# Optimization experiments

Hardware: AMD Instinct MI355X
Metric: run time of the kernel (lower is better)

The kernel has to match this reference:

```python
import jax, jax.numpy as jnp
import numpy as np

N_NODES = 100000
N_EDGES = 600000
D = 128
H = 256


def setup_inputs() -> dict:
    key = jax.random.key(0)
    ks = jax.random.split(key, 8)
    nodes = jax.random.normal(ks[0], (N_NODES, D), dtype=jnp.float32)
    senders = jax.random.randint(ks[1], (N_EDGES,), 0, N_NODES)
    receivers = jax.random.randint(ks[2], (N_EDGES,), 0, N_NODES)
    s = 0.05
    return {
        "nodes": nodes,
        "senders": senders,
        "receivers": receivers,
        "Wm1": jax.random.normal(ks[3], (D, H), dtype=jnp.float32) * s,
        "bm1": jnp.zeros((H,), dtype=jnp.float32),
        "Wm2": jax.random.normal(ks[4], (H, D), dtype=jnp.float32) * s,
        "bm2": jnp.zeros((D,), dtype=jnp.float32),
        "Wn1": jax.random.normal(ks[5], (2 * D, H), dtype=jnp.float32) * s,
        "bn1": jnp.zeros((H,), dtype=jnp.float32),
        "Wn2": jax.random.normal(ks[6], (H, D), dtype=jnp.float32) * s,
        "bn2": jnp.zeros((D,), dtype=jnp.float32),
    }


def reference(nodes, senders, receivers, Wm1, bm1, Wm2, bm2, Wn1, bn1, Wn2, bn2):
    # message MLP applied per node (vmap(message_fn) over nodes)
    m = jax.nn.relu(nodes @ Wm1 + bm1) @ Wm2 + bm2            # [N, D]
    # gather messages along edges by sender, segment_sum to receivers
    agg = jax.ops.segment_sum(m[senders], receivers, num_segments=nodes.shape[0])  # [N, D]
    # node update MLP on [nodes || aggregated messages]
    h = jnp.concatenate([nodes, agg], axis=-1)                # [N, 2D]
    upd = jax.nn.relu(h @ Wn1 + bn1) @ Wn2 + bn2              # [N, D]
    # residual add
    return nodes + upd
```

## Files before the change

### kernel.cpp

```cpp
#include <hip/hip_runtime.h>
#include <hip/hip_bf16.h>

#define NN 100000
#define DD 128
#define HH 256
#define NE 600000
#define CAP 32

typedef short bf8 __attribute__((ext_vector_type(8)));
typedef float f32x4 __attribute__((ext_vector_type(4)));
typedef unsigned short u16x8 __attribute__((ext_vector_type(8)));

__device__ __forceinline__ unsigned short f2bf(float f) {
  unsigned int u = __builtin_bit_cast(unsigned int, f);
  u += 0x7fffu + ((u >> 16) & 1u);
  return (unsigned short)(u >> 16);
}
__device__ __forceinline__ float bf2f(unsigned short h) {
  unsigned int u = ((unsigned int)h) << 16;
  return __builtin_bit_cast(float, u);
}

__global__ __launch_bounds__(256) void prep(
    const float* __restrict__ Wm1, const float* __restrict__ Wm2,
    const float* __restrict__ Wn1, const float* __restrict__ Wn2,
    unsigned short* __restrict__ Pm1, unsigned short* __restrict__ Pm2,
    unsigned short* __restrict__ Pn1, unsigned short* __restrict__ Pn2,
    int* __restrict__ cnt) {
  int b = blockIdx.x;
  for (int i = b * 256 + threadIdx.x; i < NN; i += 80 * 256) cnt[i] = 0;

  const float* W; unsigned short* P; int K, N, base;
  if (b < 16)      { W = Wm1; P = Pm1; K = 128; N = 256; base = 0;  }
  else if (b < 32) { W = Wm2; P = Pm2; K = 256; N = 128; base = 16; }
  else if (b < 64) { W = Wn1; P = Pn1; K = 256; N = 256; base = 32; }
  else             { W = Wn2; P = Pn2; K = 256; N = 128; base = 64; }
  int idx = (b - base) * 256 + threadIdx.x;
  int KT = K >> 5;
  int lane = idx & 63;
  int t = idx >> 6;
  int kt = t % KT, nt = t / KT;
  int n = nt * 16 + (lane & 15);
  int k0 = kt * 32 + (lane >> 4) * 8;
  unsigned short* dst = P + (size_t)idx * 8;
#pragma unroll
  for (int j = 0; j < 8; ++j) dst[j] = f2bf(W[(size_t)(k0 + j) * N + n]);
}

__global__ __launch_bounds__(512) void msg_mlp(
    const float* __restrict__ nodes, unsigned short* __restrict__ Xb,
    const unsigned short* __restrict__ W1p, const float* __restrict__ b1,
    const unsigned short* __restrict__ W2p, const float* __restrict__ b2,
    unsigned short* __restrict__ Mb,
    const int* __restrict__ snd, const int* __restrict__ rcv,
    int* __restrict__ cnt, int* __restrict__ ebuf) {
  __shared__ __align__(16) unsigned short h[64][264];
  const int row0 = blockIdx.x * 64;
  const int tid = threadIdx.x;
  const int lane = tid & 63, wave = tid >> 6;
  const int l15 = lane & 15, l4 = lane >> 4;

  {
    int e = blockIdx.x * 512 + tid;
    if (e < NE) {
      int r = rcv[e];
      int pos = atomicAdd(&cnt[r], 1);
      if (pos < CAP) ebuf[r * CAP + pos] = snd[e];
    }
  }

#pragma unroll
  for (int i = 0; i < 4; ++i) {
    int flat = (i * 512 + tid) * 4;
    int r = flat >> 7, c = flat & 127;
    float4 v = make_float4(0.f, 0.f, 0.f, 0.f);
    bool ok = (row0 + r < NN);
    if (ok) v = *(const float4*)(nodes + (size_t)(row0 + r) * DD + c);
    ushort4 o;
    o.x = f2bf(v.x); o.y = f2bf(v.y); o.z = f2bf(v.z); o.w = f2bf(v.w);
    *(ushort4*)&h[r][c] = o;
    if (ok) *(ushort4*)(Xb + (size_t)(row0 + r) * DD + c) = o;
  }
  __syncthreads();

  f32x4 acc[2][4];
#pragma unroll
  for (int mt = 0; mt < 2; ++mt)
#pragma unroll
    for (int nt = 0; nt < 4; ++nt) acc[mt][nt] = (f32x4){0.f, 0.f, 0.f, 0.f};
#pragma unroll
  for (int kt = 0; kt < 4; ++kt) {
    bf8 wfr[2], xfr[4];
#pragma unroll
    for (int mt = 0; mt < 2; ++mt) {
      int Htile = wave * 2 + mt;
      wfr[mt] = *(const bf8*)(W1p + ((size_t)(Htile * 4 + kt) * 64 + lane) * 8);
    }
#pragma unroll
    for (int nt = 0; nt < 4; ++nt)
      xfr[nt] = *(const bf8*)&h[nt * 16 + l15][kt * 32 + l4 * 8];
#pragma unroll
    for (int mt = 0; mt < 2; ++mt)
#pragma unroll
      for (int nt = 0; nt < 4; ++nt)
        acc[mt][nt] = __builtin_amdgcn_mfma_f32_16x16x32_bf16(wfr[mt], xfr[nt], acc[mt][nt], 0, 0, 0);
  }
  __syncthreads();

#pragma unroll
  for (int mt = 0; mt < 2; ++mt) {
    int Hbase = wave * 32 + mt * 16 + l4 * 4;
    float4 bv = *(const float4*)(b1 + Hbase);
#pragma unroll
    for (int nt = 0; nt < 4; ++nt) {
      ushort4 o;
      float v0 = acc[mt][nt][0] + bv.x; o.x = f2bf(v0 > 0.f ? v0 : 0.f);
      float v1 = acc[mt][nt][1] + bv.y; o.y = f2bf(v1 > 0.f ? v1 : 0.f);
      float v2 = acc[mt][nt][2] + bv.z; o.z = f2bf(v2 > 0.f ? v2 : 0.f);
      float v3 = acc[mt][nt][3] + bv.w; o.w = f2bf(v3 > 0.f ? v3 : 0.f);
      *(ushort4*)&h[nt * 16 + l15][Hbase] = o;
    }
  }
  __syncthreads();

  f32x4 acc2[4];
#pragma unroll
  for (int nt = 0; nt < 4; ++nt) acc2[nt] = (f32x4){0.f, 0.f, 0.f, 0.f};
#pragma unroll
  for (int kt = 0; kt < 8; ++kt) {
    bf8 wfr, xfr[4];
    wfr = *(const bf8*)(W2p + ((size_t)(wave * 8 + kt) * 64 + lane) * 8);
#pragma unroll
    for (int nt = 0; nt < 4; ++nt)
      xfr[nt] = *(const bf8*)&h[nt * 16 + l15][kt * 32 + l4 * 8];
#pragma unroll
    for (int nt = 0; nt < 4; ++nt)
      acc2[nt] = __builtin_amdgcn_mfma_f32_16x16x32_bf16(wfr, xfr[nt], acc2[nt], 0, 0, 0);
  }
  {
    int Dbase = wave * 16 + l4 * 4;
    float4 bv = *(const float4*)(b2 + Dbase);
#pragma unroll
    for (int nt = 0; nt < 4; ++nt) {
      int node = row0 + nt * 16 + l15;
      if (node < NN) {
        ushort4 o;
        o.x = f2bf(acc2[nt][0] + bv.x);
        o.y = f2bf(acc2[nt][1] + bv.y);
        o.z = f2bf(acc2[nt][2] + bv.z);
        o.w = f2bf(acc2[nt][3] + bv.w);
        *(ushort4*)(Mb + (size_t)node * DD + Dbase) = o;
      }
    }
  }
}

__global__ __launch_bounds__(256) void gather(
    const unsigned short* __restrict__ Mb, const int* __restrict__ ebuf,
    const int* __restrict__ cnt, unsigned short* __restrict__ aggb) {
  int node = blockIdx.x * 4 + (threadIdx.x >> 6);
  if (node >= NN) return;
  int lane = threadIdx.x & 63;
  int deg = cnt[node];
  deg = (deg < CAP) ? deg : CAP;
  const int base_e = node * CAP;
  float a0 = 0.f, a1 = 0.f;
  for (int b = 0; b < deg; b += 8) {
    int s[8];
    ushort2 mv[8];
#pragma unroll
    for (int u = 0; u < 8; ++u) s[u] = ebuf[base_e + b + u];
#pragma unroll
    for (int u = 0; u < 8; ++u) {
      int sl = s[u];
      sl = (sl < 0) ? 0 : sl;
      sl = (sl >= NN) ? 0 : sl;
      mv[u] = *(const ushort2*)(Mb + (size_t)sl * DD + lane * 2);
    }
#pragma unroll
    for (int u = 0; u < 8; ++u) {
      bool act = (b + u) < deg;
      a0 += act ? bf2f(mv[u].x) : 0.f;
      a1 += act ? bf2f(mv[u].y) : 0.f;
    }
  }
  ushort2 o;
  o.x = f2bf(a0);
  o.y = f2bf(a1);
  *(ushort2*)(aggb + (size_t)node * DD + lane * 2) = o;
}

__global__ __launch_bounds__(512) void node_mlp(
    const unsigned short* __restrict__ Xb, const unsigned short* __restrict__ aggb,
    const unsigned short* __restrict__ W1p, const float* __restrict__ b1,
    const unsigned short* __restrict__ W2p, const float* __restrict__ b2,
    float* __restrict__ out) {
  __shared__ __align__(16) unsigned short h[64][264];
  const int row0 = blockIdx.x * 64;
  const int tid = threadIdx.x;
  const int lane = tid & 63, wave = tid >> 6;
  const int l15 = lane & 15, l4 = lane >> 4;

#pragma unroll
  for (int i = 0; i < 2; ++i) {
    int flat = (i * 512 + tid) * 8;
    int r = flat >> 7, c = flat & 127;
    u16x8 v = (u16x8)0;
    if (row0 + r < NN) v = *(const u16x8*)(Xb + (size_t)(row0 + r) * DD + c);
    *(u16x8*)&h[r][c] = v;
  }
#pragma unroll
  for (int i = 0; i < 2; ++i) {
    int flat = (i * 512 + tid) * 8;
    int r = flat >> 7, c = flat & 127;
    u16x8 v = (u16x8)0;
    if (row0 + r < NN) v = *(const u16x8*)(aggb + (size_t)(row0 + r) * DD + c);
    *(u16x8*)&h[r][128 + c] = v;
  }
  __syncthreads();

  ushort4 resid[4];
  {
    int Dbase = wave * 16 + l4 * 4;
#pragma unroll
    for (int nt = 0; nt < 4; ++nt)
      resid[nt] = *(ushort4*)&h[nt * 16 + l15][Dbase];
  }

  f32x4 acc[2][4];
#pragma unroll
  for (int mt = 0; mt < 2; ++mt)
#pragma unroll
    for (int nt = 0; nt < 4; ++nt) acc[mt][nt] = (f32x4){0.f, 0.f, 0.f, 0.f};
#pragma unroll
  for (int kt = 0; kt < 8; ++kt) {
    bf8 wfr[2], xfr[4];
#pragma unroll
    for (int mt = 0; mt < 2; ++mt) {
      int Htile = wave * 2 + mt;
      wfr[mt] = *(const bf8*)(W1p + ((size_t)(Htile * 8 + kt) * 64 + lane) * 8);
    }
#pragma unroll
    for (int nt = 0; nt < 4; ++nt)
      xfr[nt] = *(const bf8*)&h[nt * 16 + l15][kt * 32 + l4 * 8];
#pragma unroll
    for (int mt = 0; mt < 2; ++mt)
#pragma unroll
      for (int nt = 0; nt < 4; ++nt)
        acc[mt][nt] = __builtin_amdgcn_mfma_f32_16x16x32_bf16(wfr[mt], xfr[nt], acc[mt][nt], 0, 0, 0);
  }
  __syncthreads();

#pragma unroll
  for (int mt = 0; mt < 2; ++mt) {
    int Hbase = wave * 32 + mt * 16 + l4 * 4;
    float4 bv = *(const float4*)(b1 + Hbase);
#pragma unroll
    for (int nt = 0; nt < 4; ++nt) {
      ushort4 o;
      float v0 = acc[mt][nt][0] + bv.x; o.x = f2bf(v0 > 0.f ? v0 : 0.f);
      float v1 = acc[mt][nt][1] + bv.y; o.y = f2bf(v1 > 0.f ? v1 : 0.f);
      float v2 = acc[mt][nt][2] + bv.z; o.z = f2bf(v2 > 0.f ? v2 : 0.f);
      float v3 = acc[mt][nt][3] + bv.w; o.w = f2bf(v3 > 0.f ? v3 : 0.f);
      *(ushort4*)&h[nt * 16 + l15][Hbase] = o;
    }
  }
  __syncthreads();

  f32x4 acc2[4];
#pragma unroll
  for (int nt = 0; nt < 4; ++nt) acc2[nt] = (f32x4){0.f, 0.f, 0.f, 0.f};
#pragma unroll
  for (int kt = 0; kt < 8; ++kt) {
    bf8 wfr, xfr[4];
    wfr = *(const bf8*)(W2p + ((size_t)(wave * 8 + kt) * 64 + lane) * 8);
#pragma unroll
    for (int nt = 0; nt < 4; ++nt)
      xfr[nt] = *(const bf8*)&h[nt * 16 + l15][kt * 32 + l4 * 8];
#pragma unroll
    for (int nt = 0; nt < 4; ++nt)
      acc2[nt] = __builtin_amdgcn_mfma_f32_16x16x32_bf16(wfr, xfr[nt], acc2[nt], 0, 0, 0);
  }
  {
    int Dbase = wave * 16 + l4 * 4;
    float4 bv = *(const float4*)(b2 + Dbase);
#pragma unroll
    for (int nt = 0; nt < 4; ++nt) {
      int node = row0 + nt * 16 + l15;
      if (node < NN) {
        float4 o;
        o.x = bf2f(resid[nt].x) + acc2[nt][0] + bv.x;
        o.y = bf2f(resid[nt].y) + acc2[nt][1] + bv.y;
        o.z = bf2f(resid[nt].z) + acc2[nt][2] + bv.z;
        o.w = bf2f(resid[nt].w) + acc2[nt][3] + bv.w;
        *(float4*)(out + (size_t)node * DD + Dbase) = o;
      }
    }
  }
}

extern "C" void kernel_launch(void* const* d_in, const int* in_sizes, int n_in,
                              void* d_out, int out_size, void* d_ws, size_t ws_size,
                              hipStream_t stream) {
  const float* nodes = (const float*)d_in[0];
  const int* senders = (const int*)d_in[1];
  const int* receivers = (const int*)d_in[2];
  const float* Wm1 = (const float*)d_in[3];
  const float* bm1 = (const float*)d_in[4];
  const float* Wm2 = (const float*)d_in[5];
  const float* bm2 = (const float*)d_in[6];
  const float* Wn1 = (const float*)d_in[7];
  const float* bn1 = (const float*)d_in[8];
  const float* Wn2 = (const float*)d_in[9];
  const float* bn2 = (const float*)d_in[10];
  float* out = (float*)d_out;

  char* ws = (char*)d_ws;
  unsigned short* Xb   = (unsigned short*)(ws);
  unsigned short* Mb   = (unsigned short*)(ws + 25600000);
  unsigned short* aggb = (unsigned short*)(ws + 51200000);
  int* cnt    = (int*)(ws + 76800000);
  int* ebuf   = (int*)(ws + 77200000);
  unsigned short* Wm1p = (unsigned short*)(ws + 90000000);
  unsigned short* Wm2p = (unsigned short*)(ws + 90065536);
  unsigned short* Wn1p = (unsigned short*)(ws + 90131072);
  unsigned short* Wn2p = (unsigned short*)(ws + 90262144);

  prep<<<80, 256, 0, stream>>>(Wm1, Wm2, Wn1, Wn2, Wm1p, Wm2p, Wn1p, Wn2p, cnt);
  msg_mlp<<<1563, 512, 0, stream>>>(nodes, Xb, Wm1p, bm1, Wm2p, bm2, Mb,
                                    senders, receivers, cnt, ebuf);
  gather<<<25000, 256, 0, stream>>>(Mb, ebuf, cnt, aggb);
  node_mlp<<<1563, 512, 0, stream>>>(Xb, aggb, Wn1p, bn1, Wn2p, bn2, out);
}
```

Measured before the change: 242.7 us.

## Fuse neighbor gather into node MLP and move edge bucketing after message MLP

Removes the separate gather kernel and the aggb intermediate buffer: each wave of node_mlp now sums the bf16 messages of its 8 rows directly into shared memory before the GEMMs. The edge-bucketing atomics in msg_mlp are moved to the end of the kernel so they overlap with or follow the MLP work, and node_mlp gets an occupancy hint of 4 blocks. This saves one launch and a 25.6MB write plus re-read. In exchange, the gather latency now sits serially in front of the MFMA work inside each block, which depends on occupancy to hide it.

```diff
diff --git a/kernel.cpp b/kernel.cpp
--- a/kernel.cpp
+++ b/kernel.cpp
@@ -60,15 +60,6 @@
   const int lane = tid & 63, wave = tid >> 6;
   const int l15 = lane & 15, l4 = lane >> 4;
 
-  {
-    int e = blockIdx.x * 512 + tid;
-    if (e < NE) {
-      int r = rcv[e];
-      int pos = atomicAdd(&cnt[r], 1);
-      if (pos < CAP) ebuf[r * CAP + pos] = snd[e];
-    }
-  }
-
 #pragma unroll
   for (int i = 0; i < 4; ++i) {
     int flat = (i * 512 + tid) * 4;
@@ -153,45 +144,20 @@
       }
     }
   }
-}
-
-__global__ __launch_bounds__(256) void gather(
-    const unsigned short* __restrict__ Mb, const int* __restrict__ ebuf,
-    const int* __restrict__ cnt, unsigned short* __restrict__ aggb) {
-  int node = blockIdx.x * 4 + (threadIdx.x >> 6);
-  if (node >= NN) return;
-  int lane = threadIdx.x & 63;
-  int deg = cnt[node];
-  deg = (deg < CAP) ? deg : CAP;
-  const int base_e = node * CAP;
-  float a0 = 0.f, a1 = 0.f;
-  for (int b = 0; b < deg; b += 8) {
-    int s[8];
-    ushort2 mv[8];
-#pragma unroll
-    for (int u = 0; u < 8; ++u) s[u] = ebuf[base_e + b + u];
-#pragma unroll
-    for (int u = 0; u < 8; ++u) {
-      int sl = s[u];
-      sl = (sl < 0) ? 0 : sl;
-      sl = (sl >= NN) ? 0 : sl;
-      mv[u] = *(const ushort2*)(Mb + (size_t)sl * DD + lane * 2);
-    }
-#pragma unroll
-    for (int u = 0; u < 8; ++u) {
-      bool act = (b + u) < deg;
-      a0 += act ? bf2f(mv[u].x) : 0.f;
-      a1 += act ? bf2f(mv[u].y) : 0.f;
-    }
-  }
-  ushort2 o;
-  o.x = f2bf(a0);
-  o.y = f2bf(a1);
-  *(ushort2*)(aggb + (size_t)node * DD + lane * 2) = o;
-}
-
-__global__ __launch_bounds__(512) void node_mlp(
-    const unsigned short* __restrict__ Xb, const unsigned short* __restrict__ aggb,
+
+  {
+    int e = blockIdx.x * 512 + tid;
+    if (e < NE) {
+      int r = rcv[e];
+      int pos = atomicAdd(&cnt[r], 1);
+      if (pos < CAP) ebuf[r * CAP + pos] = snd[e];
+    }
+  }
+}
+
+__global__ __launch_bounds__(512, 4) void node_mlp(
+    const unsigned short* __restrict__ Xb, const unsigned short* __restrict__ Mb,
+    const int* __restrict__ ebuf, const int* __restrict__ cnt,
     const unsigned short* __restrict__ W1p, const float* __restrict__ b1,
     const unsigned short* __restrict__ W2p, const float* __restrict__ b2,
     float* __restrict__ out) {
@@ -209,13 +175,40 @@
     if (row0 + r < NN) v = *(const u16x8*)(Xb + (size_t)(row0 + r) * DD + c);
     *(u16x8*)&h[r][c] = v;
   }
-#pragma unroll
-  for (int i = 0; i < 2; ++i) {
-    int flat = (i * 512 + tid) * 8;
-    int r = flat >> 7, c = flat & 127;
-    u16x8 v = (u16x8)0;
-    if (row0 + r < NN) v = *(const u16x8*)(aggb + (size_t)(row0 + r) * DD + c);
-    *(u16x8*)&h[r][128 + c] = v;
+
+#pragma unroll 1
+  for (int q = 0; q < 8; ++q) {
+    int r = wave * 8 + q;
+    int node = row0 + r;
+    float a0 = 0.f, a1 = 0.f;
+    if (node < NN) {
+      int deg = cnt[node];
+      deg = (deg < CAP) ? deg : CAP;
+      const int base_e = node * CAP;
+      for (int b = 0; b < deg; b += 8) {
+        int s[8];
+        ushort2 mv[8];
+#pragma unroll
+        for (int u = 0; u < 8; ++u) s[u] = ebuf[base_e + b + u];
+#pragma unroll
+        for (int u = 0; u < 8; ++u) {
+          int sl = s[u];
+          sl = (sl < 0) ? 0 : sl;
+          sl = (sl >= NN) ? 0 : sl;
+          mv[u] = *(const ushort2*)(Mb + (size_t)sl * DD + lane * 2);
+        }
+#pragma unroll
+        for (int u = 0; u < 8; ++u) {
+          bool act = (b + u) < deg;
+          a0 += act ? bf2f(mv[u].x) : 0.f;
+          a1 += act ? bf2f(mv[u].y) : 0.f;
+        }
+      }
+    }
+    ushort2 o;
+    o.x = f2bf(a0);
+    o.y = f2bf(a1);
+    *(ushort2*)&h[r][128 + lane * 2] = o;
   }
   __syncthreads();
 
@@ -318,17 +311,16 @@
   char* ws = (char*)d_ws;
   unsigned short* Xb   = (unsigned short*)(ws);
   unsigned short* Mb   = (unsigned short*)(ws + 25600000);
-  unsigned short* aggb = (unsigned short*)(ws + 51200000);
-  int* cnt    = (int*)(ws + 76800000);
-  int* ebuf   = (int*)(ws + 77200000);
-  unsigned short* Wm1p = (unsigned short*)(ws + 90000000);
-  unsigned short* Wm2p = (unsigned short*)(ws + 90065536);
-  unsigned short* Wn1p = (unsigned short*)(ws + 90131072);
-  unsigned short* Wn2p = (unsigned short*)(ws + 90262144);
+  int* cnt    = (int*)(ws + 51200000);
+  int* ebuf   = (int*)(ws + 51600000);
+  unsigned short* Wm1p = (unsigned short*)(ws + 64400000);
+  unsigned short* Wm2p = (unsigned short*)(ws + 64465536);
+  unsigned short* Wn1p = (unsigned short*)(ws + 64531072);
+  unsigned short* Wn2p = (unsigned short*)(ws + 64662144);
 
   prep<<<80, 256, 0, stream>>>(Wm1, Wm2, Wn1, Wn2, Wm1p, Wm2p, Wn1p, Wn2p, cnt);
   msg_mlp<<<1563, 512, 0, stream>>>(nodes, Xb, Wm1p, bm1, Wm2p, bm2, Mb,
                                     senders, receivers, cnt, ebuf);
-  gather<<<25000, 256, 0, stream>>>(Mb, ebuf, cnt, aggb);
-  node_mlp<<<1563, 512, 0, stream>>>(Xb, aggb, Wn1p, bn1, Wn2p, bn2, out);
-}
+  node_mlp<<<1563, 512, 0, stream>>>(Xb, Mb, ebuf, cnt,
+                                     Wn1p, bn1, Wn2p, bn2, out);
+}
```

After: 253.1 us. +4.3%, slower.
